# Kernel tuning notes

Measured on AMD Instinct MI355X. Metric: run time of the kernel, lower is better.

## Reference

```python
import jax, jax.numpy as jnp
import numpy as np

C = 256

def _conv1x1(x, w, b):
    # x: [B,C,H,W], w: [O,I], b: [O]  (1x1 conv == pointwise GEMM over channels)
    return jnp.einsum('oi,bihw->bohw', w, x) + b[None, :, None, None]

def setup_inputs() -> dict:
    key = jax.random.key(0)
    ks = jax.random.split(key, 9)
    s = 1.0 / np.sqrt(C)
    x = jax.random.normal(ks[0], (16, C, 64, 64), dtype=jnp.float32)
    wf = jax.random.uniform(ks[1], (C, C), jnp.float32, -s, s)
    bf = jax.random.uniform(ks[2], (C,), jnp.float32, -s, s)
    wg = jax.random.uniform(ks[3], (C, C), jnp.float32, -s, s)
    bg = jax.random.uniform(ks[4], (C,), jnp.float32, -s, s)
    wh = jax.random.uniform(ks[5], (C, C), jnp.float32, -s, s)
    bh = jax.random.uniform(ks[6], (C,), jnp.float32, -s, s)
    wv = jax.random.uniform(ks[7], (C, C), jnp.float32, -s, s)
    bv = jax.random.uniform(ks[8], (C,), jnp.float32, -s, s)
    return {"x": x, "wf": wf, "bf": bf, "wg": wg, "bg": bg,
            "wh": wh, "bh": bh, "wv": wv, "bv": bv}

def reference(x, wf, bf, wg, bg, wh, bh, wv, bv):
    fx = _conv1x1(x, wf, bf)              # [B,C,H,W]
    gx = _conv1x1(x, wg, bg)              # [B,C,H,W]
    # scores: fx^T @ gx over spatial H -> [B,C,W,W]
    scores = jnp.einsum('bchw,bchv->bcwv', fx, gx)
    attn = jax.nn.softmax(scores, axis=-1)  # softmax over last W dim
    hx = _conv1x1(x, wh, bh)              # [B,C,H,W]
    out = jnp.einsum('bchw,bcwv->bchv', hx, attn)  # hx @ attn -> [B,C,H,W]
    return _conv1x1(out, wv, bv)
```

## Files before the change

### kernel.cpp

```cpp
#include <hip/hip_runtime.h>
#include <math.h>

#define CH  256
#define SPA 4096
#define BB  16
#define PLANE 16777216

typedef _Float16 f16x8 __attribute__((ext_vector_type(8)));
typedef _Float16 f16x4 __attribute__((ext_vector_type(4)));
typedef float    f32x4 __attribute__((ext_vector_type(4)));

__device__ __forceinline__ void gload16(const void* g, void* l) {
    __builtin_amdgcn_global_load_lds(
        (const __attribute__((address_space(1))) unsigned int*)g,
        (__attribute__((address_space(3))) unsigned int*)l, 16, 0, 0);
}

__global__ __launch_bounds__(256) void xpose_kernel(
    const float* __restrict__ src, _Float16* __restrict__ dst)
{
    __shared__ float T[64][65];
    const int t  = threadIdx.x;
    const int b  = blockIdx.x >> 8;
    const int st = (blockIdx.x >> 2) & 63;
    const int rt = blockIdx.x & 3;
    const int s0 = st << 6, r0 = rt << 6;

    #pragma unroll
    for (int p = 0; p < 4; ++p) {
        int k = (t >> 4) + (p << 4);
        float4 v = *(const float4*)(src + (((size_t)((b << 8) + r0 + k)) << 12)
                                        + s0 + ((t & 15) << 2));
        T[k][((t & 15) << 2) + 0] = v.x;
        T[k][((t & 15) << 2) + 1] = v.y;
        T[k][((t & 15) << 2) + 2] = v.z;
        T[k][((t & 15) << 2) + 3] = v.w;
    }
    __syncthreads();

    const int s  = t >> 2;
    const int kg = (t & 3) << 4;
    const size_t obase = (((size_t)((b << 12) + s0 + s)) << 8) + r0 + kg;

    f16x8 h0, h1;
    #pragma unroll
    for (int i = 0; i < 16; ++i) {
        _Float16 hv = (_Float16)T[kg + i][s];
        if (i < 8) h0[i] = hv; else h1[i - 8] = hv;
    }
    *(f16x8*)(dst + obase)     = h0;
    *(f16x8*)(dst + obase + 8) = h1;
}

__global__ __launch_bounds__(256) void cpose_kernel(
    const _Float16* __restrict__ src, _Float16* __restrict__ dst)
{
    __shared__ _Float16 T[64][68];
    const int t  = threadIdx.x;
    const int b  = blockIdx.x >> 8;
    const int st = (blockIdx.x >> 2) & 63;
    const int ct = blockIdx.x & 3;
    const int s0 = st << 6, c0 = ct << 6;

    #pragma unroll
    for (int p = 0; p < 4; ++p) {
        int fi = (p << 8) + t;
        int r = fi >> 4, s4 = (fi & 15) << 2;
        f16x4 v = *(const f16x4*)(src + (((size_t)((b << 8) + c0 + r)) << 12) + s0 + s4);
        *(f16x4*)&T[r][s4] = v;
    }
    __syncthreads();

    const int s  = t >> 2;
    const int cg = (t & 3) << 4;
    f16x8 h0, h1;
    #pragma unroll
    for (int i = 0; i < 16; ++i) {
        _Float16 hv = T[cg + i][s];
        if (i < 8) h0[i] = hv; else h1[i - 8] = hv;
    }
    const size_t obase = (((size_t)((b << 12) + s0 + s)) << 8) + c0 + cg;
    *(f16x8*)(dst + obase)     = h0;
    *(f16x8*)(dst + obase + 8) = h1;
}

__global__ __launch_bounds__(256) void wcvt_kernel(
    const float* __restrict__ w0, const float* __restrict__ w1,
    const float* __restrict__ w2, const float* __restrict__ w3,
    _Float16* __restrict__ dst)
{
    const int idx = blockIdx.x * 256 + threadIdx.x;
    dst[idx]             = (_Float16)w0[idx];
    dst[65536 + idx]     = (_Float16)w1[idx];
    dst[131072 + idx]    = (_Float16)w2[idx];
    dst[196608 + idx]    = (_Float16)w3[idx];
}

__global__ __launch_bounds__(256, 4) void gemm_fgh_kernel(
    const _Float16* __restrict__ xT, const _Float16* __restrict__ wc,
    const float* __restrict__ bias0, const float* __restrict__ bias1,
    const float* __restrict__ bias2, _Float16* __restrict__ outp)
{
    __shared__ _Float16 S[2][8192];

    const int tid = threadIdx.x;
    const int w = tid >> 6, lane = tid & 63, q = lane >> 4, li = lane & 15;
    const int wx = w & 1, wy = w >> 1;

    const int r_ = ((blockIdx.x & 7) << 9) + (blockIdx.x >> 3);
    const int ot    = r_ & 3;
    const int stile = (r_ >> 2) & 63;
    const int b     = r_ >> 8;
    const int s0 = stile << 6, o0 = ot << 6;

    const float* biases[3] = {bias0, bias1, bias2};

    f32x4 acc[3][2][2];
    #pragma unroll
    for (int m = 0; m < 3; ++m)
        #pragma unroll
        for (int t2 = 0; t2 < 2; ++t2)
            #pragma unroll
            for (int u = 0; u < 2; ++u) acc[m][t2][u] = (f32x4){0.f, 0.f, 0.f, 0.f};

    const int rr = tid >> 2;
    const int cs = (((tid & 3) ^ ((rr >> 1) & 3)) << 3);
    const int sw = (li >> 1) & 3;

    auto STAGE = [&](_Float16* sA, int kb) {
        const size_t ga = (((size_t)((b << 12) + s0 + rr)) << 8) + kb + cs;
        gload16(xT + ga, sA + tid * 8);
        #pragma unroll
        for (int m = 0; m < 3; ++m) {
            const size_t gb = (((size_t)(o0 + rr)) << 8) + m * 65536 + kb + cs;
            gload16(wc + gb, sA + 2048 + m * 2048 + tid * 8);
        }
    };

    auto COMPUTE = [&](const _Float16* sA) {
        f16x8 a[2];
        #pragma unroll
        for (int t2 = 0; t2 < 2; ++t2)
            a[t2] = *(const f16x8*)(sA + (((wy << 5) + (t2 << 4) + li) * 32) + ((q ^ sw) << 3));
        #pragma unroll
        for (int m = 0; m < 3; ++m) {
            const _Float16* sB = sA + 2048 + m * 2048;
            f16x8 b0 = *(const f16x8*)(sB + (((wx << 5) + li) * 32) + ((q ^ sw) << 3));
            f16x8 b1 = *(const f16x8*)(sB + (((wx << 5) + 16 + li) * 32) + ((q ^ sw) << 3));
            #pragma unroll
            for (int t2 = 0; t2 < 2; ++t2) {
                acc[m][t2][0] = __builtin_amdgcn_mfma_f32_16x16x32_f16(a[t2], b0, acc[m][t2][0], 0, 0, 0);
                acc[m][t2][1] = __builtin_amdgcn_mfma_f32_16x16x32_f16(a[t2], b1, acc[m][t2][1], 0, 0, 0);
            }
        }
    };

    STAGE(S[0], 0);

    #pragma unroll 1
    for (int ks = 0; ks < 7; ++ks) {
        STAGE(S[(ks + 1) & 1], (ks + 1) << 5);
        asm volatile("s_waitcnt vmcnt(4)" ::: "memory");
        __builtin_amdgcn_s_barrier();
        COMPUTE(S[ks & 1]);
        asm volatile("s_waitcnt lgkmcnt(0)" ::: "memory");
        __builtin_amdgcn_s_barrier();
    }
    asm volatile("s_waitcnt vmcnt(0)" ::: "memory");
    __builtin_amdgcn_s_barrier();
    COMPUTE(S[1]);

    _Float16* Lr = &S[0][0];
    __syncthreads();
    #pragma unroll
    for (int m = 0; m < 3; ++m) {
        #pragma unroll
        for (int u = 0; u < 2; ++u) {
            const int o = (wx << 5) + (u << 4) + li;
            const float bz = biases[m][o0 + o];
            #pragma unroll
            for (int t2 = 0; t2 < 2; ++t2) {
                const int s = (wy << 5) + (t2 << 4) + (q << 2);
                f32x4 v = acc[m][t2][u];
                f16x4 pv;
                pv[0] = (_Float16)(v[0] + bz); pv[1] = (_Float16)(v[1] + bz);
                pv[2] = (_Float16)(v[2] + bz); pv[3] = (_Float16)(v[3] + bz);
                *(f16x4*)&Lr[m * 4608 + o * 72 + s] = pv;
            }
        }
    }
    __syncthreads();
    #pragma unroll
    for (int m = 0; m < 3; ++m) {
        _Float16* ob = outp + (size_t)m * PLANE;
        #pragma unroll
        for (int it = 0; it < 2; ++it) {
            const int idx = (it << 8) + tid;
            const int row = idx >> 3, c8 = (idx & 7) << 3;
            f16x8 hv = *(const f16x8*)&Lr[m * 4608 + row * 72 + c8];
            *(f16x8*)(ob + (((size_t)((b << 8) + o0 + row)) << 12) + s0 + c8) = hv;
        }
    }
}

__global__ __launch_bounds__(256) void gemm16_kernel(
    const _Float16* __restrict__ xT, const _Float16* __restrict__ wp,
    const float* __restrict__ bias, float* __restrict__ outp)
{
    __shared__ _Float16 S[2][8192];

    const int tid = threadIdx.x;
    const int w = tid >> 6, lane = tid & 63, quad = lane >> 4, li = lane & 15;
    const int wx = w & 1, wy = w >> 1;

    const int r_ = ((blockIdx.x & 7) << 7) + (blockIdx.x >> 3);
    const int ot    = r_ & 1;
    const int stile = (r_ >> 1) & 31;
    const int b     = r_ >> 6;
    const int s0 = stile << 7, o0 = ot << 7;

    f32x4 acc[4][4];
    #pragma unroll
    for (int t2 = 0; t2 < 4; ++t2)
        #pragma unroll
        for (int u = 0; u < 4; ++u) acc[t2][u] = (f32x4){0.f, 0.f, 0.f, 0.f};

    const int rr = lane >> 2;
    const int cs = (((lane & 3) ^ ((rr >> 1) & 3)) << 3);
    const int sw = (li >> 1) & 3;

    auto STAGE = [&](_Float16* sAB, int kb) {
        #pragma unroll
        for (int j = 0; j < 32; j += 16) {
            const int r = (w << 5) + j + rr;
            const size_t ga = (((size_t)((b << 12) + s0 + r)) << 8) + kb + cs;
            const size_t gb = ((size_t)(o0 + r) << 8) + kb + cs;
            const int lo_ = ((w << 5) + j) * 32 + lane * 8;
            gload16(xT + ga, sAB + lo_);
            gload16(wp + gb, sAB + 4096 + lo_);
        }
    };

    auto COMPUTE = [&](const _Float16* sAB) {
        f16x8 a[4], bfr[4];
        #pragma unroll
        for (int t2 = 0; t2 < 4; ++t2) {
            a[t2]   = *(const f16x8*)(sAB + ((wy << 6) + (t2 << 4) + li) * 32 + ((quad ^ sw) << 3));
            bfr[t2] = *(const f16x8*)(sAB + 4096 + ((wx << 6) + (t2 << 4) + li) * 32 + ((quad ^ sw) << 3));
        }
        #pragma unroll
        for (int t2 = 0; t2 < 4; ++t2)
            #pragma unroll
            for (int u = 0; u < 4; ++u)
                acc[t2][u] = __builtin_amdgcn_mfma_f32_16x16x32_f16(a[t2], bfr[u], acc[t2][u], 0, 0, 0);
    };

    STAGE(S[0], 0);

    #pragma unroll 1
    for (int ks = 0; ks < 7; ++ks) {
        STAGE(S[(ks + 1) & 1], (ks + 1) << 5);
        asm volatile("s_waitcnt vmcnt(4)" ::: "memory");
        __builtin_amdgcn_s_barrier();
        COMPUTE(S[ks & 1]);
        asm volatile("s_waitcnt lgkmcnt(0)" ::: "memory");
        __builtin_amdgcn_s_barrier();
    }
    asm volatile("s_waitcnt vmcnt(0)" ::: "memory");
    __builtin_amdgcn_s_barrier();
    COMPUTE(S[1]);

    float* Lf = (float*)&S[0][0];
    #pragma unroll
    for (int h = 0; h < 2; ++h) {
        __syncthreads();
        if (wx == h) {
            #pragma unroll
            for (int u = 0; u < 4; ++u) {
                const int r = (u << 4) + li;
                const float bz = bias[o0 + (h << 6) + r];
                #pragma unroll
                for (int t2 = 0; t2 < 4; ++t2) {
                    const int s = (wy << 6) + (t2 << 4) + (quad << 2);
                    f32x4 v = acc[t2][u];
                    f32x4 pv = {v[0] + bz, v[1] + bz, v[2] + bz, v[3] + bz};
                    *(f32x4*)&Lf[r * 128 + (s ^ ((r & 7) << 2))] = pv;
                }
            }
        }
        __syncthreads();
        #pragma unroll
        for (int it = 0; it < 8; ++it) {
            const int idx = (it << 8) + tid;
            const int row = idx >> 5, c4 = (idx & 31) << 2;
            f32x4 v = *(const f32x4*)&Lf[row * 128 + (c4 ^ ((row & 7) << 2))];
            float4 pv = {v[0], v[1], v[2], v[3]};
            *(float4*)(outp + (((size_t)((b << 8) + o0 + (h << 6) + row)) << 12) + s0 + c4) = pv;
        }
    }
}

__global__ __launch_bounds__(256) void attn_mfma_kernel(
    const _Float16* __restrict__ fx, const _Float16* __restrict__ gx,
    const _Float16* __restrict__ hx, _Float16* __restrict__ ob)
{
    __shared__ _Float16 L[23040];
    const int FT = 0, GT = 4608, HM = 9216;
    const int FR = 13824, GR = 18432;
    const int PT = 13824;

    const int t = threadIdx.x;
    const int wave = t >> 6, lane = t & 63, q = lane >> 4, li = lane & 15;
    const int bc = blockIdx.x;
    const _Float16* Fp = fx + (size_t)bc * SPA;
    const _Float16* Gp = gx + (size_t)bc * SPA;
    const _Float16* Hp = hx + (size_t)bc * SPA;
    _Float16* Op = ob + (size_t)bc * SPA;

    #pragma unroll
    for (int p = 0; p < 2; ++p) {
        int ci = t + (p << 8);
        int h = ci >> 3, w8 = (ci & 7) << 3;
        *(f16x8*)&L[FR + h * 72 + w8] = *(const f16x8*)(Fp + h * 64 + w8);
        *(f16x8*)&L[GR + h * 72 + w8] = *(const f16x8*)(Gp + h * 64 + w8);
        *(f16x8*)&L[HM + h * 72 + w8] = *(const f16x8*)(Hp + h * 64 + w8);
    }
    __syncthreads();

    {
        const int src = (wave < 2) ? FR : GR;
        const int dst = (wave < 2) ? FT : GT;
        const int mtb = (wave & 1) << 1;
        f16x8 id0, id1;
        #pragma unroll
        for (int j = 0; j < 8; ++j) {
            id0[j] = (_Float16)(((q << 3) + j == li)      ? 1.0f : 0.0f);
            id1[j] = (_Float16)(((q << 3) + j == li + 16) ? 1.0f : 0.0f);
        }
        #pragma unroll
        for (int mi = 0; mi < 2; ++mi) {
            const int mt = mtb + mi;
            f16x8 a0 = *(const f16x8*)&L[src + (mt * 16 + li) * 72 + (q << 3)];
            f16x8 a1 = *(const f16x8*)&L[src + (mt * 16 + li) * 72 + 32 + (q << 3)];
            #pragma unroll
            for (int nt = 0; nt < 4; ++nt) {
                f32x4 d = {0.f, 0.f, 0.f, 0.f};
                d = __builtin_amdgcn_mfma_f32_16x16x32_f16(
                        (nt < 2) ? a0 : a1, (nt & 1) ? id1 : id0, d, 0, 0, 0);
                f16x4 e;
                e[0] = (_Float16)d[0]; e[1] = (_Float16)d[1];
                e[2] = (_Float16)d[2]; e[3] = (_Float16)d[3];
                *(f16x4*)&L[dst + (nt * 16 + li) * 72 + mt * 16 + (q << 2)] = e;
            }
        }
    }
    __syncthreads();

    {
        f16x8 a0 = *(const f16x8*)&L[FT + (wave * 16 + li) * 72 + (q << 3)];
        f16x8 a1 = *(const f16x8*)&L[FT + (wave * 16 + li) * 72 + 32 + (q << 3)];
        f32x4 s_[4];
        #pragma unroll
        for (int nt = 0; nt < 4; ++nt) {
            f16x8 b0 = *(const f16x8*)&L[GT + (nt * 16 + li) * 72 + (q << 3)];
            f16x8 b1 = *(const f16x8*)&L[GT + (nt * 16 + li) * 72 + 32 + (q << 3)];
            f32x4 acc = {0.f, 0.f, 0.f, 0.f};
            acc = __builtin_amdgcn_mfma_f32_16x16x32_f16(a0, b0, acc, 0, 0, 0);
            acc = __builtin_amdgcn_mfma_f32_16x16x32_f16(a1, b1, acc, 0, 0, 0);
            s_[nt] = acc;
        }
        float mx[4], sm[4];
        #pragma unroll
        for (int r = 0; r < 4; ++r) {
            float m0 = fmaxf(fmaxf(s_[0][r], s_[1][r]), fmaxf(s_[2][r], s_[3][r]));
            m0 = fmaxf(m0, __shfl_xor(m0, 1));
            m0 = fmaxf(m0, __shfl_xor(m0, 2));
            m0 = fmaxf(m0, __shfl_xor(m0, 4));
            m0 = fmaxf(m0, __shfl_xor(m0, 8));
            mx[r] = m0;
        }
        #pragma unroll
        for (int nt = 0; nt < 4; ++nt)
            #pragma unroll
            for (int r = 0; r < 4; ++r)
                s_[nt][r] = __expf(s_[nt][r] - mx[r]);
        #pragma unroll
        for (int r = 0; r < 4; ++r) {
            float s0 = (s_[0][r] + s_[1][r]) + (s_[2][r] + s_[3][r]);
            s0 += __shfl_xor(s0, 1);
            s0 += __shfl_xor(s0, 2);
            s0 += __shfl_xor(s0, 4);
            s0 += __shfl_xor(s0, 8);
            sm[r] = 1.f / s0;
        }
        #pragma unroll
        for (int nt = 0; nt < 4; ++nt) {
            const int v  = nt * 16 + li;
            const int sw = ((v >> 3) & 7) << 3;
            #pragma unroll
            for (int r = 0; r < 4; ++r) {
                const int w = wave * 16 + (q << 2) + r;
                L[PT + v * 72 + (w ^ sw)] = (_Float16)(s_[nt][r] * sm[r]);
            }
        }
    }
    __syncthreads();

    {
        f16x8 a0 = *(const f16x8*)&L[HM + (wave * 16 + li) * 72 + (q << 3)];
        f16x8 a1 = *(const f16x8*)&L[HM + (wave * 16 + li) * 72 + 32 + (q << 3)];
        #pragma unroll
        for (int nt = 0; nt < 4; ++nt) {
            const int v  = nt * 16 + li;
            const int sw = ((v >> 3) & 7) << 3;
            f16x8 b0 = *(const f16x8*)&L[PT + v * 72 + ((q << 3) ^ sw)];
            f16x8 b1 = *(const f16x8*)&L[PT + v * 72 + ((32 + (q << 3)) ^ sw)];
            f32x4 acc = {0.f, 0.f, 0.f, 0.f};
            acc = __builtin_amdgcn_mfma_f32_16x16x32_f16(a0, b0, acc, 0, 0, 0);
            acc = __builtin_amdgcn_mfma_f32_16x16x32_f16(a1, b1, acc, 0, 0, 0);
            #pragma unroll
            for (int r = 0; r < 4; ++r)
                Op[(wave * 16 + (q << 2) + r) * 64 + v] = (_Float16)acc[r];
        }
    }
}

extern "C" void kernel_launch(void* const* d_in, const int* in_sizes, int n_in,
                              void* d_out, int out_size, void* d_ws, size_t ws_size,
                              hipStream_t stream)
{
    const float* x  = (const float*)d_in[0];
    const float* wf = (const float*)d_in[1];
    const float* bf = (const float*)d_in[2];
    const float* wg = (const float*)d_in[3];
    const float* bg = (const float*)d_in[4];
    const float* wh = (const float*)d_in[5];
    const float* bh = (const float*)d_in[6];
    const float* wv = (const float*)d_in[7];
    const float* bv = (const float*)d_in[8];

    char* base = (char*)d_ws;
    const size_t MB = 1ull << 20;
    _Float16* xT  = (_Float16*)base;
    _Float16* fxb = (_Float16*)(base + 32 * MB);
    _Float16* ob  = (_Float16*)(base + 128 * MB);
    _Float16* obT = (_Float16*)base;
    _Float16* wc  = (_Float16*)(base + 160 * MB);

    _Float16* gxb = fxb + PLANE;
    _Float16* hxb = gxb + PLANE;

    dim3 blk(256);
    xpose_kernel<<<4096, blk, 0, stream>>>(x, xT);
    wcvt_kernel<<<256, blk, 0, stream>>>(wf, wg, wh, wv, wc);

    gemm_fgh_kernel<<<4096, blk, 0, stream>>>(xT, wc, bf, bg, bh, fxb);

    attn_mfma_kernel<<<4096, blk, 0, stream>>>(fxb, gxb, hxb, ob);

    cpose_kernel<<<4096, blk, 0, stream>>>(ob, obT);

    gemm16_kernel<<<1024, blk, 0, stream>>>(obT, wc + 196608, bv, (float*)d_out);
}
```

Before: 245.2 us.

## Write attention output in channel-blocked layout and drop transpose kernel

The attention kernel now writes its output directly in a layout of [batch][channel group of 8][spatial][8 channels], and the final projection GEMM reads 16-byte chunks from that layout. This removes the separate cpose transpose kernel and its 32 MB round trip through memory. Blocks are remapped so that the 8 channels of a group land in neighbouring blocks, but each thread's output store is a scalar 2-byte write at a stride of 16 bytes. That could hurt write coalescing unless the L2 cache merges the partial writes.

```diff
diff --git a/kernel.cpp b/kernel.cpp
--- a/kernel.cpp
+++ b/kernel.cpp
@@ -52,38 +52,6 @@
     *(f16x8*)(dst + obase + 8) = h1;
 }
 
-__global__ __launch_bounds__(256) void cpose_kernel(
-    const _Float16* __restrict__ src, _Float16* __restrict__ dst)
-{
-    __shared__ _Float16 T[64][68];
-    const int t  = threadIdx.x;
-    const int b  = blockIdx.x >> 8;
-    const int st = (blockIdx.x >> 2) & 63;
-    const int ct = blockIdx.x & 3;
-    const int s0 = st << 6, c0 = ct << 6;
-
-    #pragma unroll
-    for (int p = 0; p < 4; ++p) {
-        int fi = (p << 8) + t;
-        int r = fi >> 4, s4 = (fi & 15) << 2;
-        f16x4 v = *(const f16x4*)(src + (((size_t)((b << 8) + c0 + r)) << 12) + s0 + s4);
-        *(f16x4*)&T[r][s4] = v;
-    }
-    __syncthreads();
-
-    const int s  = t >> 2;
-    const int cg = (t & 3) << 4;
-    f16x8 h0, h1;
-    #pragma unroll
-    for (int i = 0; i < 16; ++i) {
-        _Float16 hv = T[cg + i][s];
-        if (i < 8) h0[i] = hv; else h1[i - 8] = hv;
-    }
-    const size_t obase = (((size_t)((b << 12) + s0 + s)) << 8) + c0 + cg;
-    *(f16x8*)(dst + obase)     = h0;
-    *(f16x8*)(dst + obase + 8) = h1;
-}
-
 __global__ __launch_bounds__(256) void wcvt_kernel(
     const float* __restrict__ w0, const float* __restrict__ w1,
     const float* __restrict__ w2, const float* __restrict__ w3,
@@ -204,7 +172,7 @@
 }
 
 __global__ __launch_bounds__(256) void gemm16_kernel(
-    const _Float16* __restrict__ xT, const _Float16* __restrict__ wp,
+    const _Float16* __restrict__ obt, const _Float16* __restrict__ wp,
     const float* __restrict__ bias, float* __restrict__ outp)
 {
     __shared__ _Float16 S[2][8192];
@@ -227,16 +195,18 @@
 
     const int rr = lane >> 2;
     const int cs = (((lane & 3) ^ ((rr >> 1) & 3)) << 3);
+    const int cc = cs >> 3;
     const int sw = (li >> 1) & 3;
 
     auto STAGE = [&](_Float16* sAB, int kb) {
         #pragma unroll
         for (int j = 0; j < 32; j += 16) {
             const int r = (w << 5) + j + rr;
-            const size_t ga = (((size_t)((b << 12) + s0 + r)) << 8) + kb + cs;
+            const size_t ga = (((size_t)((b << 5) + (kb >> 3) + cc)) * 4096
+                               + s0 + r) * 8;
             const size_t gb = ((size_t)(o0 + r) << 8) + kb + cs;
             const int lo_ = ((w << 5) + j) * 32 + lane * 8;
-            gload16(xT + ga, sAB + lo_);
+            gload16(obt + ga, sAB + lo_);
             gload16(wp + gb, sAB + 4096 + lo_);
         }
     };
@@ -302,7 +272,7 @@
 
 __global__ __launch_bounds__(256) void attn_mfma_kernel(
     const _Float16* __restrict__ fx, const _Float16* __restrict__ gx,
-    const _Float16* __restrict__ hx, _Float16* __restrict__ ob)
+    const _Float16* __restrict__ hx, _Float16* __restrict__ obt)
 {
     __shared__ _Float16 L[23040];
     const int FT = 0, GT = 4608, HM = 9216;
@@ -311,16 +281,24 @@
 
     const int t = threadIdx.x;
     const int wave = t >> 6, lane = t & 63, q = lane >> 4, li = lane & 15;
-    const int bc = blockIdx.x;
+
+    const int bid = blockIdx.x;
+    const int x  = bid & 7, X = bid >> 3;
+    const int gi = (x << 6) + (X >> 3);
+    const int ci = X & 7;
+    const int b  = gi >> 5, g = gi & 31;
+    const int c  = (g << 3) + ci;
+    const int bc = (b << 8) + c;
+
     const _Float16* Fp = fx + (size_t)bc * SPA;
     const _Float16* Gp = gx + (size_t)bc * SPA;
     const _Float16* Hp = hx + (size_t)bc * SPA;
-    _Float16* Op = ob + (size_t)bc * SPA;
+    _Float16* Opt = obt + ((size_t)((b << 5) + g)) * 32768 + ci;
 
     #pragma unroll
     for (int p = 0; p < 2; ++p) {
-        int ci = t + (p << 8);
-        int h = ci >> 3, w8 = (ci & 7) << 3;
+        int ci_ = t + (p << 8);
+        int h = ci_ >> 3, w8 = (ci_ & 7) << 3;
         *(f16x8*)&L[FR + h * 72 + w8] = *(const f16x8*)(Fp + h * 64 + w8);
         *(f16x8*)&L[GR + h * 72 + w8] = *(const f16x8*)(Gp + h * 64 + w8);
         *(f16x8*)&L[HM + h * 72 + w8] = *(const f16x8*)(Hp + h * 64 + w8);
@@ -419,8 +397,10 @@
             acc = __builtin_amdgcn_mfma_f32_16x16x32_f16(a0, b0, acc, 0, 0, 0);
             acc = __builtin_amdgcn_mfma_f32_16x16x32_f16(a1, b1, acc, 0, 0, 0);
             #pragma unroll
-            for (int r = 0; r < 4; ++r)
-                Op[(wave * 16 + (q << 2) + r) * 64 + v] = (_Float16)acc[r];
+            for (int r = 0; r < 4; ++r) {
+                const int s = (wave * 16 + (q << 2) + r) * 64 + v;
+                Opt[(size_t)s * 8] = (_Float16)acc[r];
+            }
         }
     }
 }
@@ -443,8 +423,7 @@
     const size_t MB = 1ull << 20;
     _Float16* xT  = (_Float16*)base;
     _Float16* fxb = (_Float16*)(base + 32 * MB);
-    _Float16* ob  = (_Float16*)(base + 128 * MB);
-    _Float16* obT = (_Float16*)base;
+    _Float16* obt = (_Float16*)(base + 128 * MB);
     _Float16* wc  = (_Float16*)(base + 160 * MB);
 
     _Float16* gxb = fxb + PLANE;
@@ -456,9 +435,7 @@
 
     gemm_fgh_kernel<<<4096, blk, 0, stream>>>(xT, wc, bf, bg, bh, fxb);
 
-    attn_mfma_kernel<<<4096, blk, 0, stream>>>(fxb, gxb, hxb, ob);
-
-    cpose_kernel<<<4096, blk, 0, stream>>>(ob, obT);
-
-    gemm16_kernel<<<1024, blk, 0, stream>>>(obT, wc + 196608, bv, (float*)d_out);
-}
+    attn_mfma_kernel<<<4096, blk, 0, stream>>>(fxb, gxb, hxb, obt);
+
+    gemm16_kernel<<<1024, blk, 0, stream>>>(obt, wc + 196608, bv, (float*)d_out);
+}
```

Measured after the change: 247.2 us. About the same (+0.8%).
